# Kernel tuning notes

Hardware: AMD Instinct MI355X
Metric: run time of the kernel (lower is better)

The kernel has to match this reference:

```python
import jax, jax.numpy as jnp
import numpy as np

N_SLOTS = 32


def entmax15(z):
    """Exact 1.5-entmax along last axis (Peters et al. 2019 closed form)."""
    x = z / 2.0
    x = x - jnp.max(x, axis=-1, keepdims=True)
    zs = jnp.flip(jnp.sort(x, axis=-1), axis=-1)  # descending
    n = zs.shape[-1]
    k = jnp.arange(1, n + 1, dtype=zs.dtype)
    mean = jnp.cumsum(zs, axis=-1) / k
    meansq = jnp.cumsum(zs * zs, axis=-1) / k
    ss = k * (meansq - mean * mean)
    delta = (1.0 - ss) / k
    tau = mean - jnp.sqrt(jnp.maximum(delta, 0.0))
    support = jnp.sum(tau <= zs, axis=-1) - 1  # index of last valid k
    tau_star = jnp.take_along_axis(tau, support[..., None], axis=-1)
    p = jnp.maximum(x - tau_star, 0.0)
    return p * p


def dual_memory_scan(x_seq, W_h, W_x, b_h, W_write, n_slots):
    """E25 entmax dual-memory recurrence. x_seq: [B,T,D]."""
    B, T, D = x_seq.shape
    scale = 1.0 / jnp.sqrt(jnp.array(D, dtype=x_seq.dtype))
    tape0 = jnp.zeros((B, n_slots, D), dtype=x_seq.dtype)
    work0 = jnp.zeros((B, D), dtype=x_seq.dtype)
    # precompute input projection for all timesteps
    xw = jnp.einsum('btd,ed->bte', x_seq, W_x)  # [B,T,D]

    def step(carry, x_t):
        tape, work = carry
        h_pre = work @ W_h.T + x_t + b_h                    # [B,D]
        # entmax read over tape slots
        r_scores = jnp.einsum('bnd,bd->bn', tape, h_pre) * scale
        a = entmax15(r_scores)                              # [B,n]
        read = jnp.einsum('bn,bnd->bd', a, tape)
        h_new = jnp.tanh(h_pre + read)                      # [B,D]
        # entmax write back to tape
        w_val = h_new @ W_write.T                           # [B,D]
        w_scores = jnp.einsum('bnd,bd->bn', tape, h_new) * scale
        b = entmax15(w_scores)                              # [B,n]
        tape_new = tape + b[..., None] * (w_val[:, None, :] - tape)
        return (tape_new, h_new), h_new

    (tape_f, work_f), hs = jax.lax.scan(step, (tape0, work0), jnp.swapaxes(xw, 0, 1))
    out = jnp.swapaxes(hs, 0, 1)  # [B,T,D]
    return out, tape_f, work_f


def setup_inputs() -> dict:
    key = jax.random.key(0)
    ks = jax.random.split(key, 7)
    B, T, D = 8, 1024, 512
    s = 0.02
    return {
        'x': jax.random.normal(ks[0], (B, T, D), dtype=jnp.float32),
        'W_in': jax.random.normal(ks[1], (2 * D, D), dtype=jnp.float32) * s,
        'W_out': jax.random.normal(ks[2], (D, D), dtype=jnp.float32) * s,
        'W_h': jax.random.normal(ks[3], (D, D), dtype=jnp.float32) * s,
        'W_x': jax.random.normal(ks[4], (D, D), dtype=jnp.float32) * s,
        'b_h': jnp.zeros((D,), dtype=jnp.float32),
        'W_write': jax.random.normal(ks[5], (D, D), dtype=jnp.float32) * s,
    }


def reference(x, W_in, W_out, W_h, W_x, b_h, W_write):
    d_inner = W_out.shape[1]
    xz = x @ W_in.T                                   # [B,T,2*d_inner]
    x_proj, z = xz[..., :d_inner], xz[..., d_inner:]
    x_proj = jax.nn.silu(x_proj)
    out, tape_f, work_f = dual_memory_scan(x_proj, W_h, W_x, b_h, W_write, N_SLOTS)
    out = out * jax.nn.silu(z)
    out = out @ W_out.T
    return out, tape_f, work_f
```

## Files before the change

kernel.cpp:

```cpp
#include <hip/hip_runtime.h>


#define BB 8
#define TT 1024
#define DD 512
#define NS 32
#define KW 8
#define SLOTS 1288

static constexpr float SCALE = 0.044194173824159216f;

__device__ __forceinline__ float siluf(float v) { return v / (1.0f + __expf(-v)); }

template <int CTRL>
__device__ __forceinline__ float dpp_add(float x) {
  int xi = __builtin_bit_cast(int, x);
  int yi = __builtin_amdgcn_update_dpp(0, xi, CTRL, 0xF, 0xF, false);
  return x + __builtin_bit_cast(float, yi);
}
template <int PAT>
__device__ __forceinline__ float swz_add(float x) {
  int yi = __builtin_amdgcn_ds_swizzle(__builtin_bit_cast(int, x), PAT);
  return x + __builtin_bit_cast(float, yi);
}
template <int J>
__device__ __forceinline__ float xlane(float x) {
  if constexpr (J == 1) {
    int yi = __builtin_amdgcn_update_dpp(0, __builtin_bit_cast(int, x), 0xB1, 0xF, 0xF, false);
    return __builtin_bit_cast(float, yi);
  } else if constexpr (J == 2) {
    int yi = __builtin_amdgcn_update_dpp(0, __builtin_bit_cast(int, x), 0x4E, 0xF, 0xF, false);
    return __builtin_bit_cast(float, yi);
  } else {
    int yi = __builtin_amdgcn_ds_swizzle(__builtin_bit_cast(int, x), (J << 10) | 0x1F);
    return __builtin_bit_cast(float, yi);
  }
}
__device__ __forceinline__ float reduce8(float x) {
  x = swz_add<0x041F>(x);
  x = swz_add<0x081F>(x);
  x = swz_add<0x101F>(x);
  return x;
}
__device__ __forceinline__ float reduce32(float x) {
  x = dpp_add<0x121>(x);
  x = dpp_add<0x122>(x);
  x = dpp_add<0x124>(x);
  x = dpp_add<0x128>(x);
  return swz_add<0x401F>(x);
}

__device__ __forceinline__ float entmax32(float z, int l32) {
  float x = 0.5f * z;
  float m = x;
  m = fmaxf(m, xlane<1>(m));  m = fmaxf(m, xlane<2>(m));
  m = fmaxf(m, xlane<4>(m));  m = fmaxf(m, xlane<8>(m));
  m = fmaxf(m, xlane<16>(m));
  x -= m;
  float s = x;
#define XST(K, J) { float y = xlane<J>(s); bool up = (((l32 & K) == 0) ^ ((l32 & J) == 0)); s = up ? fminf(s, y) : fmaxf(s, y); }
  XST(2, 1)
  XST(4, 2)  XST(4, 1)
  XST(8, 4)  XST(8, 2)  XST(8, 1)
  XST(16, 8) XST(16, 4) XST(16, 2) XST(16, 1)
  XST(32, 16) XST(32, 8) XST(32, 4) XST(32, 2) XST(32, 1)
#undef XST
  float cs = s, cq = s * s;
  #pragma unroll
  for (int d = 1; d < 32; d <<= 1) {
    float ts = __shfl_up(cs, d, 32);
    float tq = __shfl_up(cq, d, 32);
    if (l32 >= d) { cs += ts; cq += tq; }
  }
  float kf    = (float)(l32 + 1);
  float mean  = cs / kf;
  float msq   = cq / kf;
  float ssv   = kf * (msq - mean * mean);
  float delta = (1.0f - ssv) / kf;
  float tau   = mean - sqrtf(fmaxf(delta, 0.0f));
  unsigned long long mask = __ballot(tau <= s);
  int support = __popcll(mask & 0xFFFFFFFFull) - 1;
  float tau_star = __shfl(tau, support, 32);
  float p = fmaxf(x - tau_star, 0.0f);
  return p * p;
}

__device__ __forceinline__ void pubv(unsigned long long* p, int t, float v) {
  unsigned long long u = ((unsigned long long)(unsigned)(t + 1) << 32) |
                         (unsigned long long)__builtin_bit_cast(unsigned, v);
  __hip_atomic_store(p, u, __ATOMIC_RELAXED, __HIP_MEMORY_SCOPE_AGENT);
}
__device__ __forceinline__ float pollv(const unsigned long long* p, int t) {
  const unsigned want = (unsigned)(t + 1);
  unsigned long long u;
  do {
    u = __hip_atomic_load(p, __ATOMIC_RELAXED, __HIP_MEMORY_SCOPE_AGENT);
  } while ((unsigned)(u >> 32) != want);
  return __builtin_bit_cast(float, (unsigned)(u & 0xFFFFFFFFu));
}

template <int MODE>
__global__ __launch_bounds__(256) void gemm_tn(const float* __restrict__ A,
                                               const float* __restrict__ Bm,
                                               float* __restrict__ C0,
                                               float* __restrict__ C1,
                                               int M, int N, int K) {
  const int bm = blockIdx.x, bn = blockIdx.y;
  const int tid = threadIdx.x;
  const int tx = tid & 15, ty = tid >> 4;
  __shared__ __align__(16) float As[16][132];
  __shared__ __align__(16) float Bs[16][132];
  float acc[8][8] = {};
  const int rowA0 = bm * 128, rowB0 = bn * 128;

  for (int k0 = 0; k0 < K; k0 += 16) {
    #pragma unroll
    for (int q = 0; q < 2; ++q) {
      int idx = tid + q * 256;
      int r   = idx >> 2;
      int kq  = (idx & 3) * 4;
      float4 a4 = *(const float4*)&A [(size_t)(rowA0 + r) * K + k0 + kq];
      float4 b4 = *(const float4*)&Bm[(size_t)(rowB0 + r) * K + k0 + kq];
      As[kq + 0][r] = a4.x; As[kq + 1][r] = a4.y; As[kq + 2][r] = a4.z; As[kq + 3][r] = a4.w;
      Bs[kq + 0][r] = b4.x; Bs[kq + 1][r] = b4.y; Bs[kq + 2][r] = b4.z; Bs[kq + 3][r] = b4.w;
    }
    __syncthreads();
    #pragma unroll
    for (int kk = 0; kk < 16; ++kk) {
      float4 a0 = *(const float4*)&As[kk][ty * 8];
      float4 a1 = *(const float4*)&As[kk][ty * 8 + 4];
      float4 b0 = *(const float4*)&Bs[kk][tx * 8];
      float4 b1 = *(const float4*)&Bs[kk][tx * 8 + 4];
      float av[8] = {a0.x, a0.y, a0.z, a0.w, a1.x, a1.y, a1.z, a1.w};
      float bv[8] = {b0.x, b0.y, b0.z, b0.w, b1.x, b1.y, b1.z, b1.w};
      #pragma unroll
      for (int i = 0; i < 8; ++i)
        #pragma unroll
        for (int j = 0; j < 8; ++j) acc[i][j] = fmaf(av[i], bv[j], acc[i][j]);
    }
    __syncthreads();
  }
  #pragma unroll
  for (int i = 0; i < 8; ++i) {
    int gr = rowA0 + ty * 8 + i;
    #pragma unroll
    for (int j = 0; j < 8; ++j) {
      int gc = rowB0 + tx * 8 + j;
      float v = acc[i][j];
      if (MODE == 0) {
        float sv = siluf(v);
        if (gc < 512) C0[(size_t)gr * 512 + gc]         = sv;
        else          C1[(size_t)gr * 512 + (gc - 512)] = sv;
      } else {
        C0[(size_t)gr * N + gc] = v;
      }
    }
  }
}

__global__ __launch_bounds__(1024) void scan_kernel(
    const float* __restrict__ Wh, const float* __restrict__ Ww,
    const float* __restrict__ bh, const float* __restrict__ XW,
    const float* __restrict__ SZ, float* __restrict__ Y,
    unsigned long long* __restrict__ Pp,
    float* __restrict__ outTape, float* __restrict__ outWork) {
  const int tid  = threadIdx.x;
  const int wv   = tid >> 6, lane = tid & 63;
  const int b    = blockIdx.x & 7, g = blockIdx.x >> 3;
  const int l32  = lane & 31;
  const int seg  = tid & 7;
  const int row  = tid >> 3;

  __shared__ float tape[NS][DD];
  __shared__ float h_full[DD], hpC[DD], wvvC[DD];
  __shared__ float hp_loc[64], wv_loc[64];
  __shared__ float ws_arr[NS], q1part[KW * NS], q2part[KW];
  __shared__ float bArr[NS], aArr[NS];

  float w[64];
  {
    const float* src = (row < 64) ? (Wh + (size_t)(g * 64 + row) * DD)
                                  : (Ww + (size_t)(g * 64 + row - 64) * DD);
    #pragma unroll
    for (int q = 0; q < 16; ++q) {
      int c4 = seg * 64 + ((4 * q + 4 * seg) & 63);
      float4 v4 = *(const float4*)(src + c4);
      w[4*q+0] = v4.x; w[4*q+1] = v4.y; w[4*q+2] = v4.z; w[4*q+3] = v4.w;
    }
  }
  const float bhv = (seg == 0 && row < 64) ? bh[g * 64 + row] : 0.f;
  for (int e = tid; e < NS * DD; e += 1024) ((float*)tape)[e] = 0.f;
  if (tid < DD) h_full[tid] = 0.f;
  __syncthreads();

  for (int t = 0; t <= TT; ++t) {
    unsigned long long* pbuf = Pp + ((size_t)(t & 1) * BB + b) * SLOTS;
    float xwv = 0.f;
    if (seg == 0 && row < 64 && t < TT)
      xwv = XW[((size_t)b * TT + t) * DD + g * 64 + row];
    float szv = 0.f;
    if (t < TT && tid < DD && (tid >> 6) == g)
      szv = SZ[((size_t)b * TT + t) * DD + tid];

    float pv = 0.f;
    #pragma unroll
    for (int q = 0; q < 16; ++q) {
      int c4 = seg * 64 + ((4 * q + 4 * seg) & 63);
      float4 h4 = *(const float4*)&h_full[c4];
      pv = fmaf(w[4*q+0], h4.x, pv);
      pv = fmaf(w[4*q+1], h4.y, pv);
      pv = fmaf(w[4*q+2], h4.z, pv);
      pv = fmaf(w[4*q+3], h4.w, pv);
    }
    pv = reduce8(pv);
    if (seg == 0) {
      float hv = (row < 64) ? (pv + xwv + bhv) : pv;
      if (row < 64) hp_loc[row] = hv; else wv_loc[row - 64] = hv;
      pubv(&pbuf[g * 128 + row], t, hv);
    }
    __syncthreads();

    {
      int n = wv * 2 + (lane >> 5);
      float s1 = fmaf(tape[n][g * 64 + 2 * l32],     hp_loc[2 * l32],
               tape[n][g * 64 + 2 * l32 + 1] * hp_loc[2 * l32 + 1]);
      s1 = reduce32(s1);
      if (l32 == 0) pubv(&pbuf[1024 + g * 33 + n], t, s1);
      if (wv == 0 && lane < 32) {
        float s2 = fmaf(wv_loc[l32], hp_loc[l32],
                        wv_loc[l32 + 32] * hp_loc[l32 + 32]);
        s2 = reduce32(s2);
        if (l32 == 0) pubv(&pbuf[1024 + g * 33 + 32], t, s2);
      }
    }
    {
      int n = wv * 2 + (lane >> 5);
      float sw = 0.f;
      #pragma unroll
      for (int j = 0; j < 16; ++j)
        sw = fmaf(tape[n][l32 + 32 * j], h_full[l32 + 32 * j], sw);
      sw = reduce32(sw);
      if (l32 == 0) ws_arr[n] = sw * SCALE;
    }
    __syncthreads();

    if (wv == 1) {
      float pb = entmax32(ws_arr[l32], l32);
      if (lane < NS) bArr[lane] = pb;
    }
    {
      float v = pollv(&pbuf[tid], t);
      int i = tid & 127, gg = tid >> 7;
      if (i < 64) hpC[gg * 64 + i] = v;
      else        wvvC[gg * 64 + (i - 64)] = v;
      if (tid < KW * 33) {
        float v2 = pollv(&pbuf[1024 + tid], t);
        int gg2 = tid / 33, j2 = tid - gg2 * 33;
        if (j2 < 32) q1part[gg2 * 32 + j2] = v2;
        else         q2part[gg2] = v2;
      }
    }
    __syncthreads();

    if (wv == 0) {
      if (t < TT) {
        float q1s = 0.f, q2s = 0.f;
        #pragma unroll
        for (int k = 0; k < KW; ++k) {
          q1s += q1part[k * 32 + l32];
          q2s += q2part[k];
        }
        float pb = bArr[l32];
        float rs = SCALE * fmaf(pb, q2s - q1s, q1s);
        float pa = entmax32(rs, l32);
        if (lane < NS) aArr[lane] = pa;
      }
    } else {
      for (int e = tid - 64; e < NS * DD / 4; e += 960) {
        int n = e >> 7, dq = (e & 127) * 4;
        float  bn = bArr[n];
        float4 tv = *(float4*)&tape[n][dq];
        float4 wq = *(const float4*)&wvvC[dq];
        tv.x = fmaf(bn, wq.x - tv.x, tv.x);
        tv.y = fmaf(bn, wq.y - tv.y, tv.y);
        tv.z = fmaf(bn, wq.z - tv.z, tv.z);
        tv.w = fmaf(bn, wq.w - tv.w, tv.w);
        *(float4*)&tape[n][dq] = tv;
      }
    }
    __syncthreads();

    if (t == TT) {
      if (tid < DD && (tid >> 6) == g) outWork[(size_t)b * DD + tid] = h_full[tid];
      for (int e = tid; e < NS * 64; e += 1024) {
        int n = e >> 6, d = g * 64 + (e & 63);
        outTape[((size_t)b * NS + n) * DD + d] = tape[n][d];
      }
      break;
    }
    if (tid < DD) {
      float r = 0.f;
      #pragma unroll
      for (int n = 0; n < NS; ++n) r = fmaf(aArr[n], tape[n][tid], r);
      float hn = tanhf(hpC[tid] + r);
      if ((tid >> 6) == g)
        Y[((size_t)b * TT + t) * DD + tid] = hn * szv;
      h_full[tid] = hn;
    }
    __syncthreads();
  }
}

extern "C" void kernel_launch(void* const* d_in, const int* in_sizes, int n_in,
                              void* d_out, int out_size, void* d_ws, size_t ws_size,
                              hipStream_t stream) {
  (void)in_sizes; (void)n_in; (void)out_size; (void)ws_size;
  const float* x    = (const float*)d_in[0];
  const float* W_in = (const float*)d_in[1];
  const float* W_out= (const float*)d_in[2];
  const float* W_h  = (const float*)d_in[3];
  const float* W_x  = (const float*)d_in[4];
  const float* b_h  = (const float*)d_in[5];
  const float* W_wr = (const float*)d_in[6];

  float* out     = (float*)d_out;
  float* outTape = out + (size_t)BB * TT * DD;
  float* outWork = outTape + (size_t)BB * NS * DD;

  float* wsf  = (float*)d_ws;
  float* XP   = wsf;
  float* SZ   = XP + (size_t)BB * TT * DD;
  float* XWb  = SZ + (size_t)BB * TT * DD;
  unsigned long long* Pp = (unsigned long long*)(XWb + (size_t)BB * TT * DD);

  gemm_tn<0><<<dim3(64, 8), 256, 0, stream>>>(x, W_in, XP, SZ, BB * TT, 2 * DD, DD);
  gemm_tn<1><<<dim3(64, 4), 256, 0, stream>>>(XP, W_x, XWb, nullptr, BB * TT, DD, DD);
  scan_kernel<<<64, 1024, 0, stream>>>(W_h, W_wr, b_h, XWb, SZ, XP,
                                       Pp, outTape, outWork);
  gemm_tn<1><<<dim3(64, 4), 256, 0, stream>>>(XP, W_out, out, nullptr, BB * TT, DD, DD);
}
```

Before: 5.453 ms.

## Double-buffer tape, fold read into old tape, overlap tape update with read

Keeps two tape buffers so the read step can use the pre-update tape. The read becomes an algebraic combination of old slots (weight a*(1-b)) plus the write value scaled by sum(a*b). Half the tape update then runs on waves 8-15 at the same time as the read/tanh on waves 0-7, instead of as separate phases. It also replaces the 8-lane swizzle reduction of the matvec with a shared-memory partial-sum layout, which adds a barrier, and merges the two polling loops into one. Shared memory use doubles for the tape, and the regrouped read sum may round slightly differently.

```diff
diff --git a/kernel.cpp b/kernel.cpp
--- a/kernel.cpp
+++ b/kernel.cpp
@@ -35,12 +35,6 @@
     int yi = __builtin_amdgcn_ds_swizzle(__builtin_bit_cast(int, x), (J << 10) | 0x1F);
     return __builtin_bit_cast(float, yi);
   }
-}
-__device__ __forceinline__ float reduce8(float x) {
-  x = swz_add<0x041F>(x);
-  x = swz_add<0x081F>(x);
-  x = swz_add<0x101F>(x);
-  return x;
 }
 __device__ __forceinline__ float reduce32(float x) {
   x = dpp_add<0x121>(x);
@@ -90,14 +84,6 @@
                          (unsigned long long)__builtin_bit_cast(unsigned, v);
   __hip_atomic_store(p, u, __ATOMIC_RELAXED, __HIP_MEMORY_SCOPE_AGENT);
 }
-__device__ __forceinline__ float pollv(const unsigned long long* p, int t) {
-  const unsigned want = (unsigned)(t + 1);
-  unsigned long long u;
-  do {
-    u = __hip_atomic_load(p, __ATOMIC_RELAXED, __HIP_MEMORY_SCOPE_AGENT);
-  } while ((unsigned)(u >> 32) != want);
-  return __builtin_bit_cast(float, (unsigned)(u & 0xFFFFFFFFu));
-}
 
 template <int MODE>
 __global__ __launch_bounds__(256) void gemm_tn(const float* __restrict__ A,
@@ -168,77 +154,85 @@
   const int wv   = tid >> 6, lane = tid & 63;
   const int b    = blockIdx.x & 7, g = blockIdx.x >> 3;
   const int l32  = lane & 31;
-  const int seg  = tid & 7;
-  const int row  = tid >> 3;
-
-  __shared__ float tape[NS][DD];
+  const int seg  = tid >> 7;
+  const int row  = tid & 127;
+
+  __shared__ float tapeA[NS][DD];
+  __shared__ float tapeB[NS][DD];
   __shared__ float h_full[DD], hpC[DD], wvvC[DD];
+  __shared__ float Wpart[8][128];
   __shared__ float hp_loc[64], wv_loc[64];
   __shared__ float ws_arr[NS], q1part[KW * NS], q2part[KW];
-  __shared__ float bArr[NS], aArr[NS];
+  __shared__ float bArr[NS], cArr[NS];
+  __shared__ float sSh;
 
   float w[64];
   {
-    const float* src = (row < 64) ? (Wh + (size_t)(g * 64 + row) * DD)
-                                  : (Ww + (size_t)(g * 64 + row - 64) * DD);
+    const float* src = (row < 64) ? (Wh + (size_t)(g * 64 + row) * DD + seg * 64)
+                                  : (Ww + (size_t)(g * 64 + row - 64) * DD + seg * 64);
     #pragma unroll
     for (int q = 0; q < 16; ++q) {
-      int c4 = seg * 64 + ((4 * q + 4 * seg) & 63);
-      float4 v4 = *(const float4*)(src + c4);
+      float4 v4 = *(const float4*)(src + 4 * q);
       w[4*q+0] = v4.x; w[4*q+1] = v4.y; w[4*q+2] = v4.z; w[4*q+3] = v4.w;
     }
   }
-  const float bhv = (seg == 0 && row < 64) ? bh[g * 64 + row] : 0.f;
-  for (int e = tid; e < NS * DD; e += 1024) ((float*)tape)[e] = 0.f;
+  const float bhr = (tid < 64) ? bh[g * 64 + tid] : 0.f;
+  for (int e = tid; e < NS * DD; e += 1024) {
+    ((float*)tapeA)[e] = 0.f;
+    ((float*)tapeB)[e] = 0.f;
+  }
   if (tid < DD) h_full[tid] = 0.f;
   __syncthreads();
 
   for (int t = 0; t <= TT; ++t) {
+    float (*cur)[DD] = (t & 1) ? tapeB : tapeA;
+    float (*nxt)[DD] = (t & 1) ? tapeA : tapeB;
     unsigned long long* pbuf = Pp + ((size_t)(t & 1) * BB + b) * SLOTS;
+
     float xwv = 0.f;
-    if (seg == 0 && row < 64 && t < TT)
-      xwv = XW[((size_t)b * TT + t) * DD + g * 64 + row];
+    if (tid < 64 && t < TT) xwv = XW[((size_t)b * TT + t) * DD + g * 64 + tid];
     float szv = 0.f;
     if (t < TT && tid < DD && (tid >> 6) == g)
       szv = SZ[((size_t)b * TT + t) * DD + tid];
 
-    float pv = 0.f;
+    float p = 0.f;
     #pragma unroll
     for (int q = 0; q < 16; ++q) {
-      int c4 = seg * 64 + ((4 * q + 4 * seg) & 63);
-      float4 h4 = *(const float4*)&h_full[c4];
-      pv = fmaf(w[4*q+0], h4.x, pv);
-      pv = fmaf(w[4*q+1], h4.y, pv);
-      pv = fmaf(w[4*q+2], h4.z, pv);
-      pv = fmaf(w[4*q+3], h4.w, pv);
-    }
-    pv = reduce8(pv);
-    if (seg == 0) {
-      float hv = (row < 64) ? (pv + xwv + bhv) : pv;
-      if (row < 64) hp_loc[row] = hv; else wv_loc[row - 64] = hv;
-      pubv(&pbuf[g * 128 + row], t, hv);
+      float4 h4 = *(const float4*)&h_full[seg * 64 + 4 * q];
+      p = fmaf(w[4*q+0], h4.x, p);
+      p = fmaf(w[4*q+1], h4.y, p);
+      p = fmaf(w[4*q+2], h4.z, p);
+      p = fmaf(w[4*q+3], h4.w, p);
+    }
+    Wpart[seg][row] = p;
+    __syncthreads();
+
+    if (tid < 128) {
+      float s = 0.f;
+      #pragma unroll
+      for (int k = 0; k < 8; ++k) s += Wpart[k][tid];
+      float hv = (tid < 64) ? (s + xwv + bhr) : s;
+      if (tid < 64) hp_loc[tid] = hv; else wv_loc[tid - 64] = hv;
+      pubv(&pbuf[g * 128 + tid], t, hv);
     }
     __syncthreads();
 
     {
       int n = wv * 2 + (lane >> 5);
-      float s1 = fmaf(tape[n][g * 64 + 2 * l32],     hp_loc[2 * l32],
-               tape[n][g * 64 + 2 * l32 + 1] * hp_loc[2 * l32 + 1]);
+      float s1 = fmaf(cur[n][g * 64 + 2 * l32], hp_loc[2 * l32],
+                      cur[n][g * 64 + 2 * l32 + 1] * hp_loc[2 * l32 + 1]);
       s1 = reduce32(s1);
       if (l32 == 0) pubv(&pbuf[1024 + g * 33 + n], t, s1);
-      if (wv == 0 && lane < 32) {
+      if (wv == 0) {
         float s2 = fmaf(wv_loc[l32], hp_loc[l32],
                         wv_loc[l32 + 32] * hp_loc[l32 + 32]);
         s2 = reduce32(s2);
-        if (l32 == 0) pubv(&pbuf[1024 + g * 33 + 32], t, s2);
-      }
-    }
-    {
-      int n = wv * 2 + (lane >> 5);
+        if (lane == 0) pubv(&pbuf[1024 + g * 33 + 32], t, s2);
+      }
       float sw = 0.f;
       #pragma unroll
       for (int j = 0; j < 16; ++j)
-        sw = fmaf(tape[n][l32 + 32 * j], h_full[l32 + 32 * j], sw);
+        sw = fmaf(cur[n][l32 + 32 * j], h_full[l32 + 32 * j], sw);
       sw = reduce32(sw);
       if (l32 == 0) ws_arr[n] = sw * SCALE;
     }
@@ -249,15 +243,29 @@
       if (lane < NS) bArr[lane] = pb;
     }
     {
-      float v = pollv(&pbuf[tid], t);
+      const unsigned want = (unsigned)(t + 1);
+      const bool needB = (tid < KW * 33);
+      unsigned long long uA = 0, uB = 0;
+      bool okA = false, okB = !needB;
+      do {
+        if (!okA) {
+          uA = __hip_atomic_load(&pbuf[tid], __ATOMIC_RELAXED, __HIP_MEMORY_SCOPE_AGENT);
+          okA = (unsigned)(uA >> 32) == want;
+        }
+        if (!okB) {
+          uB = __hip_atomic_load(&pbuf[1024 + tid], __ATOMIC_RELAXED, __HIP_MEMORY_SCOPE_AGENT);
+          okB = (unsigned)(uB >> 32) == want;
+        }
+      } while (!(okA && okB));
+      float vA = __builtin_bit_cast(float, (unsigned)(uA & 0xFFFFFFFFu));
       int i = tid & 127, gg = tid >> 7;
-      if (i < 64) hpC[gg * 64 + i] = v;
-      else        wvvC[gg * 64 + (i - 64)] = v;
-      if (tid < KW * 33) {
-        float v2 = pollv(&pbuf[1024 + tid], t);
+      if (i < 64) hpC[gg * 64 + i] = vA;
+      else        wvvC[gg * 64 + (i - 64)] = vA;
+      if (needB) {
+        float vB = __builtin_bit_cast(float, (unsigned)(uB & 0xFFFFFFFFu));
         int gg2 = tid / 33, j2 = tid - gg2 * 33;
-        if (j2 < 32) q1part[gg2 * 32 + j2] = v2;
-        else         q2part[gg2] = v2;
+        if (j2 < 32) q1part[gg2 * 32 + j2] = vB;
+        else         q2part[gg2] = vB;
       }
     }
     __syncthreads();
@@ -273,39 +281,70 @@
         float pb = bArr[l32];
         float rs = SCALE * fmaf(pb, q2s - q1s, q1s);
         float pa = entmax32(rs, l32);
-        if (lane < NS) aArr[lane] = pa;
+        if (lane < NS) cArr[lane] = pa * (1.0f - pb);
+        float sv = reduce32(pa * pb);
+        if (lane == 0) sSh = sv;
       }
     } else {
-      for (int e = tid - 64; e < NS * DD / 4; e += 960) {
+      for (int e = tid - 64; e < 16 * 128; e += 960) {
         int n = e >> 7, dq = (e & 127) * 4;
         float  bn = bArr[n];
-        float4 tv = *(float4*)&tape[n][dq];
+        float4 tv = *(float4*)&cur[n][dq];
         float4 wq = *(const float4*)&wvvC[dq];
         tv.x = fmaf(bn, wq.x - tv.x, tv.x);
         tv.y = fmaf(bn, wq.y - tv.y, tv.y);
         tv.z = fmaf(bn, wq.z - tv.z, tv.z);
         tv.w = fmaf(bn, wq.w - tv.w, tv.w);
-        *(float4*)&tape[n][dq] = tv;
+        *(float4*)&nxt[n][dq] = tv;
       }
     }
     __syncthreads();
 
     if (t == TT) {
+      if (wv >= 8) {
+        for (int e = tid - 512; e < 16 * 128; e += 512) {
+          int n = 16 + (e >> 7), dq = (e & 127) * 4;
+          float  bn = bArr[n];
+          float4 tv = *(float4*)&cur[n][dq];
+          float4 wq = *(const float4*)&wvvC[dq];
+          tv.x = fmaf(bn, wq.x - tv.x, tv.x);
+          tv.y = fmaf(bn, wq.y - tv.y, tv.y);
+          tv.z = fmaf(bn, wq.z - tv.z, tv.z);
+          tv.w = fmaf(bn, wq.w - tv.w, tv.w);
+          *(float4*)&nxt[n][dq] = tv;
+        }
+      }
+      __syncthreads();
       if (tid < DD && (tid >> 6) == g) outWork[(size_t)b * DD + tid] = h_full[tid];
       for (int e = tid; e < NS * 64; e += 1024) {
         int n = e >> 6, d = g * 64 + (e & 63);
-        outTape[((size_t)b * NS + n) * DD + d] = tape[n][d];
+        outTape[((size_t)b * NS + n) * DD + d] = nxt[n][d];
       }
       break;
     }
-    if (tid < DD) {
+
+    if (wv < 8) {
+      int d = tid;
       float r = 0.f;
       #pragma unroll
-      for (int n = 0; n < NS; ++n) r = fmaf(aArr[n], tape[n][tid], r);
-      float hn = tanhf(hpC[tid] + r);
-      if ((tid >> 6) == g)
-        Y[((size_t)b * TT + t) * DD + tid] = hn * szv;
-      h_full[tid] = hn;
+      for (int n = 0; n < NS; ++n) r = fmaf(cArr[n], cur[n][d], r);
+      r = fmaf(sSh, wvvC[d], r);
+      float hn = tanhf(hpC[d] + r);
+      if ((d >> 6) == g)
+        Y[((size_t)b * TT + t) * DD + d] = hn * szv;
+      h_full[d] = hn;
+    } else {
+      for (int e = tid - 512; e < 16 * 128; e += 512) {
+        int n = 16 + (e >> 7), dq = (e & 127) * 4;
+        float  bn = bArr[n];
+        float4 tv = *(float4*)&cur[n][dq];
+        float4 wq = *(const float4*)&wvvC[dq];
+        tv.x = fmaf(bn, wq.x - tv.x, tv.x);
+        tv.y = fmaf(bn, wq.y - tv.y, tv.y);
+        tv.z = fmaf(bn, wq.z - tv.z, tv.z);
+        tv.w = fmaf(bn, wq.w - tv.w, tv.w);
+        *(float4*)&nxt[n][dq] = tv;
+      }
     }
     __syncthreads();
   }
```

Result: slower. 6.144 ms (+12.7%).
